# Kernel optimization log

Measured on AMD Instinct MI355X. Metric: run time of the kernel, lower is better.

## Reference

```python
import jax, jax.numpy as jnp
import numpy as np

B, N, C = 8, 1024, 640   # frames, tokens per frame (32x32), channels
H, D = 8, 80             # heads, dim per head; inner = H*D = 640
R = 3                    # adaptive context_range (uniform, odd)
SCALE = D ** -0.5


def _window_indices(batch_size, context_range):
    """Replicates the per-sample index construction in RefAttention.forward.
    First half of the batch attends within [0, B//2-1], second within [B//2, B-1]."""
    half = batch_size // 2
    hr = (context_range - 1) // 2
    rows = []
    for i in range(batch_size):
        lo_b, hi_b = (0, half - 1) if i < half else (half, batch_size - 1)
        ci = list(range(max(lo_b, i - hr), min(hi_b, i + hr + 1)))  # arange(a, min(hi_b, i+hr+1))
        while len(ci) < context_range:
            if ci[0] > lo_b:
                ci = [ci[0] - 1] + ci
            if len(ci) < context_range and ci[-1] < hi_b:
                ci = ci + [ci[-1] + 1]
        rows.append(ci)
    return np.asarray(rows, dtype=np.int32)  # [B, R]


def setup_inputs() -> dict:
    key = jax.random.key(0)
    ks = jax.random.split(key, 6)
    inner = H * D
    x = jax.random.normal(ks[0], (B, N, C), dtype=jnp.float32)
    s = 1.0 / np.sqrt(C)
    Wq = jax.random.normal(ks[1], (inner, C), dtype=jnp.float32) * s
    Wk = jax.random.normal(ks[2], (inner, C), dtype=jnp.float32) * s
    Wv = jax.random.normal(ks[3], (inner, C), dtype=jnp.float32) * s
    Wo = jax.random.normal(ks[4], (C, inner), dtype=jnp.float32) * (1.0 / np.sqrt(inner))
    bo = jnp.zeros((C,), dtype=jnp.float32)
    ctx_idx = jnp.asarray(_window_indices(B, R))  # [B, R] int32, static window gather indices
    return {"x": x, "Wq": Wq, "Wk": Wk, "Wv": Wv, "Wo": Wo, "bo": bo, "ctx_idx": ctx_idx}


def reference(x, Wq, Wk, Wv, Wo, bo, ctx_idx):
    # projections (nn.Linear, no bias): y = x @ W^T
    q = jnp.einsum('bnc,ic->bni', x, Wq)                      # [B, N, inner]
    k = jnp.einsum('bnc,ic->bni', x, Wk)                      # context defaults to x
    v = jnp.einsum('bnc,ic->bni', x, Wv)
    # original uses k.data / v.data (detached); forward value is identical
    qh = q.reshape(B, N, H, D)
    # gather per-frame K/V windows: [B, R, N, inner] -> [B, R*N, H, D]
    kw = k[ctx_idx].reshape(B, R * N, H, D)
    vw = v[ctx_idx].reshape(B, R * N, H, D)
    sim = jnp.einsum('bnhd,bmhd->bhnm', qh, kw) * SCALE       # [B, H, N, R*N]
    attn = jax.nn.softmax(sim, axis=-1)
    out = jnp.einsum('bhnm,bmhd->bnhd', attn, vw).reshape(B, N, H * D)
    return jnp.einsum('bni,ci->bnc', out, Wo) + bo            # to_out (dropout p=0)
```

## Files before the change

### kernel.cpp

```cpp
#include <hip/hip_runtime.h>
#include <hip/hip_bf16.h>

#define BB    8
#define NNTOK 1024
#define CCH   640
#define HH    8
#define DHD   80
#define RRW   3
#define MM    (BB * NNTOK)
#define INNER 640
#define SCALE 0.111803398874989484820458954f
#define QSCALE (SCALE * 1.44269504088896340736f)

#define KSTR 88
#define VSTR 72
#define PSTR 72

typedef __bf16 bf16x8 __attribute__((ext_vector_type(8)));
typedef float  f32x4  __attribute__((ext_vector_type(4)));

__device__ __forceinline__ unsigned short f2b(float f) {
    union { float f; unsigned int u; } v; v.f = f;
    unsigned int r = v.u + 0x7fffu + ((v.u >> 16) & 1u);
    return (unsigned short)(r >> 16);
}
__device__ __forceinline__ bf16x8 zero8() {
    bf16x8 z;
#pragma unroll
    for (int i = 0; i < 8; i++) z[i] = (__bf16)0.0f;
    return z;
}
__device__ __forceinline__ f32x4 zero4() {
    f32x4 z;
#pragma unroll
    for (int i = 0; i < 4; i++) z[i] = 0.0f;
    return z;
}
__device__ __forceinline__ float fexp2(float x) {
#if __has_builtin(__builtin_amdgcn_exp2f)
    return __builtin_amdgcn_exp2f(x);
#else
    return __expf(x * 0.69314718055994530942f);
#endif
}

__global__ __launch_bounds__(256) void castk(const float* __restrict__ s,
                                             unsigned short* __restrict__ d, int n) {
    int i = (blockIdx.x * 256 + threadIdx.x) * 4;
    if (i < n) {
        float4 f = *(const float4*)(s + i);
        ushort4 o;
        o.x = f2b(f.x); o.y = f2b(f.y); o.z = f2b(f.z); o.w = f2b(f.w);
        *(ushort4*)(d + i) = o;
    }
}

__global__ __launch_bounds__(256) void castw4(
    const float* __restrict__ w0, const float* __restrict__ w1,
    const float* __restrict__ w2, const float* __restrict__ w3,
    unsigned short* __restrict__ d0, unsigned short* __restrict__ d1,
    unsigned short* __restrict__ d2, unsigned short* __restrict__ d3, int n)
{
    const float* s; unsigned short* d;
    switch (blockIdx.y) {
        case 0: s = w0; d = d0; break;
        case 1: s = w1; d = d1; break;
        case 2: s = w2; d = d2; break;
        default: s = w3; d = d3; break;
    }
    int i = (blockIdx.x * 256 + threadIdx.x) * 4;
    if (i < n) {
        float4 f = *(const float4*)(s + i);
        ushort4 o;
        o.x = f2b(f.x); o.y = f2b(f.y); o.z = f2b(f.z); o.w = f2b(f.w);
        *(ushort4*)(d + i) = o;
    }
}

__global__ __launch_bounds__(256) void proj_qkv_mfma(
    const unsigned short* __restrict__ xb,
    const unsigned short* __restrict__ wqb,
    const unsigned short* __restrict__ wkb,
    const unsigned short* __restrict__ wvb,
    unsigned short* __restrict__ q16, unsigned short* __restrict__ k16,
    unsigned short* __restrict__ vto)
{
    __shared__ __align__(16) unsigned short Xs[64 * 72];
    __shared__ __align__(16) unsigned short Wsh[64 * 72];
    const int t = threadIdx.x;
    const int wvid = t >> 6, lane = t & 63, col = lane & 15, quad = lane >> 4;
    const int m0 = blockIdx.x * 64, i0 = blockIdx.y * 64, z = blockIdx.z;
    const unsigned short* W = (z == 0) ? wqb : (z == 1) ? wkb : wvb;
    const int row = t >> 2, seg = t & 3;

    f32x4 acc[4];
#pragma unroll
    for (int nt = 0; nt < 4; nt++) acc[nt] = zero4();

    for (int kt = 0; kt < INNER; kt += 64) {
        uint4 x0 = *(const uint4*)(xb + (size_t)(m0 + row) * INNER + kt + seg * 16);
        uint4 x1 = *(const uint4*)(xb + (size_t)(m0 + row) * INNER + kt + seg * 16 + 8);
        uint4 w0 = *(const uint4*)(W  + (size_t)(i0 + row) * INNER + kt + seg * 16);
        uint4 w1 = *(const uint4*)(W  + (size_t)(i0 + row) * INNER + kt + seg * 16 + 8);
        __syncthreads();
        *(uint4*)&Xs[row * 72 + seg * 16]      = x0;
        *(uint4*)&Xs[row * 72 + seg * 16 + 8]  = x1;
        *(uint4*)&Wsh[row * 72 + seg * 16]     = w0;
        *(uint4*)&Wsh[row * 72 + seg * 16 + 8] = w1;
        __syncthreads();
#pragma unroll
        for (int kbk = 0; kbk < 2; kbk++) {
            bf16x8 af = *(const bf16x8*)&Xs[(wvid * 16 + col) * 72 + kbk * 32 + quad * 8];
#pragma unroll
            for (int nt = 0; nt < 4; nt++) {
                bf16x8 bfr = *(const bf16x8*)&Wsh[(nt * 16 + col) * 72 + kbk * 32 + quad * 8];
                acc[nt] = __builtin_amdgcn_mfma_f32_16x16x32_bf16(af, bfr, acc[nt], 0, 0, 0);
            }
        }
    }
    if (z == 0) {
#pragma unroll
        for (int nt = 0; nt < 4; nt++)
#pragma unroll
            for (int r = 0; r < 4; r++)
                q16[(size_t)(m0 + wvid * 16 + quad * 4 + r) * INNER + i0 + nt * 16 + col] = f2b(acc[nt][r] * QSCALE);
    } else if (z == 1) {
#pragma unroll
        for (int nt = 0; nt < 4; nt++)
#pragma unroll
            for (int r = 0; r < 4; r++)
                k16[(size_t)(m0 + wvid * 16 + quad * 4 + r) * INNER + i0 + nt * 16 + col] = f2b(acc[nt][r]);
    } else {
#pragma unroll
        for (int nt = 0; nt < 4; nt++) {
            int i = i0 + nt * 16 + col;
            int h = i / DHD, dd = i % DHD;
#pragma unroll
            for (int r = 0; r < 4; r++) {
                int m = m0 + wvid * 16 + quad * 4 + r;
                int bfm = m >> 10, n = m & (NNTOK - 1);
                vto[((size_t)(bfm * HH + h) * DHD + dd) * NNTOK + n] = f2b(acc[nt][r]);
            }
        }
    }
}

__global__ __launch_bounds__(512, 4) void attn_mfma8(
    const unsigned short* __restrict__ qb, const unsigned short* __restrict__ kb,
    const unsigned short* __restrict__ vt, const int* __restrict__ ctx,
    unsigned short* __restrict__ ao)
{
    __shared__ __align__(16) unsigned short Ks[2][64 * KSTR];
    __shared__ __align__(16) unsigned short Vt[2][DHD * VSTR];
    __shared__ __align__(16) unsigned short Pl[8][16 * PSTR];
    const int t = threadIdx.x;
    const int wvid = t >> 6, lane = t & 63, col = lane & 15, quad = lane >> 4;
    const int qt = blockIdx.x, h = blockIdx.y, b = blockIdx.z;

    bf16x8 qf0, qf1, qf2;
    {
        const unsigned short* qp = qb + (size_t)(b * NNTOK + qt * 128 + wvid * 16 + col) * INNER + h * DHD;
        qf0 = *(const bf16x8*)(qp + quad * 8);
        qf1 = *(const bf16x8*)(qp + 32 + quad * 8);
        qf2 = zero8();
        if (quad < 2) qf2 = *(const bf16x8*)(qp + 64 + quad * 8);
    }
    f32x4 o[5];
#pragma unroll
    for (int dt = 0; dt < 5; dt++) o[dt] = zero4();
    float lp[4];
#pragma unroll
    for (int r = 0; r < 4; r++) lp[r] = 0.0f;
    unsigned short* pw = &Pl[wvid][0];

    const int ki0 = t, ki1 = t + 512;
    const int kkey0 = ki0 / 10, kseg0 = ki0 % 10;
    const int kkey1 = ki1 / 10, kseg1 = ki1 % 10;
    const int vd0 = ki0 >> 3, vs0 = ki0 & 7;
    const int vd1 = ki1 >> 3, vs1 = ki1 & 7;

    {
        const int fr = ctx[b * RRW];
        const unsigned short* kbase = kb + (size_t)(fr * NNTOK) * INNER + h * DHD;
        const unsigned short* vbase = vt + ((size_t)(fr * HH + h) * DHD) * NNTOK;
        uint4 ka0 = *(const uint4*)(kbase + (size_t)kkey0 * INNER + kseg0 * 8);
        uint4 va0 = *(const uint4*)(vbase + (size_t)vd0 * NNTOK + vs0 * 8);
        *(uint4*)&Ks[0][kkey0 * KSTR + kseg0 * 8] = ka0;
        *(uint4*)&Vt[0][vd0 * VSTR + vs0 * 8] = va0;
        if (t < 128) {
            uint4 ka1 = *(const uint4*)(kbase + (size_t)kkey1 * INNER + kseg1 * 8);
            uint4 va1 = *(const uint4*)(vbase + (size_t)vd1 * NNTOK + vs1 * 8);
            *(uint4*)&Ks[0][kkey1 * KSTR + kseg1 * 8] = ka1;
            *(uint4*)&Vt[0][vd1 * VSTR + vs1 * 8] = va1;
        }
    }

    for (int kc = 0; kc < (RRW * NNTOK) / 64; kc++) {
        __syncthreads();

        const int kcn = (kc + 1 < 48) ? kc + 1 : 47;
        const int frn = ctx[b * RRW + (kcn >> 4)];
        const int tokn = (kcn & 15) * 64;
        const unsigned short* kbase = kb + (size_t)(frn * NNTOK + tokn) * INNER + h * DHD;
        const unsigned short* vbase = vt + ((size_t)(frn * HH + h) * DHD) * NNTOK + tokn;
        uint4 ka0 = *(const uint4*)(kbase + (size_t)kkey0 * INNER + kseg0 * 8);
        uint4 va0 = *(const uint4*)(vbase + (size_t)vd0 * NNTOK + vs0 * 8);
        uint4 ka1, va1;
        if (t < 128) {
            ka1 = *(const uint4*)(kbase + (size_t)kkey1 * INNER + kseg1 * 8);
            va1 = *(const uint4*)(vbase + (size_t)vd1 * NNTOK + vs1 * 8);
        }

        const unsigned short* ksr = &Ks[kc & 1][0];
        const unsigned short* vtr = &Vt[kc & 1][0];

        f32x4 s[4];
#pragma unroll
        for (int n0 = 0; n0 < 4; n0++) {
            const unsigned short* kp = ksr + (n0 * 16 + col) * KSTR;
            bf16x8 k0 = *(const bf16x8*)(kp + quad * 8);
            bf16x8 k1 = *(const bf16x8*)(kp + 32 + quad * 8);
            bf16x8 k2 = zero8();
            if (quad < 2) k2 = *(const bf16x8*)(kp + 64 + quad * 8);
            f32x4 sv = zero4();
            sv = __builtin_amdgcn_mfma_f32_16x16x32_bf16(qf0, k0, sv, 0, 0, 0);
            sv = __builtin_amdgcn_mfma_f32_16x16x32_bf16(qf1, k1, sv, 0, 0, 0);
            sv = __builtin_amdgcn_mfma_f32_16x16x32_bf16(qf2, k2, sv, 0, 0, 0);
            s[n0] = sv;
        }
        asm volatile("" ::: "memory");
        __bf16* pb = (__bf16*)pw;
#pragma unroll
        for (int r = 0; r < 4; r++) {
            float p0 = fexp2(s[0][r]), p1 = fexp2(s[1][r]);
            float p2 = fexp2(s[2][r]), p3 = fexp2(s[3][r]);
            lp[r] += (p0 + p1) + (p2 + p3);
            const int rowoff = (quad * 4 + r) * PSTR;
            pb[rowoff +      col] = (__bf16)p0;
            pb[rowoff + 16 + col] = (__bf16)p1;
            pb[rowoff + 32 + col] = (__bf16)p2;
            pb[rowoff + 48 + col] = (__bf16)p3;
        }
        asm volatile("s_waitcnt lgkmcnt(0)" ::: "memory");
        bf16x8 pa0 = *(const bf16x8*)(pw + col * PSTR + quad * 8);
        bf16x8 pa1 = *(const bf16x8*)(pw + col * PSTR + 32 + quad * 8);
#pragma unroll
        for (int dt = 0; dt < 5; dt++) {
            const unsigned short* vp = vtr + (dt * 16 + col) * VSTR;
            bf16x8 v0 = *(const bf16x8*)(vp + quad * 8);
            bf16x8 v1 = *(const bf16x8*)(vp + 32 + quad * 8);
            o[dt] = __builtin_amdgcn_mfma_f32_16x16x32_bf16(pa0, v0, o[dt], 0, 0, 0);
            o[dt] = __builtin_amdgcn_mfma_f32_16x16x32_bf16(pa1, v1, o[dt], 0, 0, 0);
        }
        {
            unsigned short* ksb = &Ks[(kc + 1) & 1][0];
            unsigned short* vtb = &Vt[(kc + 1) & 1][0];
            *(uint4*)&ksb[kkey0 * KSTR + kseg0 * 8] = ka0;
            *(uint4*)&vtb[vd0 * VSTR + vs0 * 8] = va0;
            if (t < 128) {
                *(uint4*)&ksb[kkey1 * KSTR + kseg1 * 8] = ka1;
                *(uint4*)&vtb[vd1 * VSTR + vs1 * 8] = va1;
            }
        }
    }
#pragma unroll
    for (int r = 0; r < 4; r++) {
        float sum = lp[r];
        sum += __shfl_xor(sum, 1);
        sum += __shfl_xor(sum, 2);
        sum += __shfl_xor(sum, 4);
        sum += __shfl_xor(sum, 8);
        lp[r] = sum;
    }
#pragma unroll
    for (int r = 0; r < 4; r++) {
        const float inv = 1.0f / lp[r];
        unsigned short* op = ao + (size_t)(b * NNTOK + qt * 128 + wvid * 16 + quad * 4 + r) * INNER + h * DHD;
#pragma unroll
        for (int dt = 0; dt < 5; dt++)
            op[dt * 16 + col] = f2b(o[dt][r] * inv);
    }
}

__global__ __launch_bounds__(256) void proj_out_mfma(
    const unsigned short* __restrict__ ab, const unsigned short* __restrict__ wob,
    const float* __restrict__ bo, float* __restrict__ out)
{
    __shared__ __align__(16) unsigned short Xs[64 * 72];
    __shared__ __align__(16) unsigned short Wsh[64 * 72];
    const int t = threadIdx.x;
    const int wvid = t >> 6, lane = t & 63, col = lane & 15, quad = lane >> 4;
    const int m0 = blockIdx.x * 64, i0 = blockIdx.y * 64;
    const int row = t >> 2, seg = t & 3;

    float bias[4];
#pragma unroll
    for (int nt = 0; nt < 4; nt++) bias[nt] = bo[i0 + nt * 16 + col];

    f32x4 acc[4];
#pragma unroll
    for (int nt = 0; nt < 4; nt++) acc[nt] = zero4();

    for (int kt = 0; kt < INNER; kt += 64) {
        uint4 x0 = *(const uint4*)(ab  + (size_t)(m0 + row) * INNER + kt + seg * 16);
        uint4 x1 = *(const uint4*)(ab  + (size_t)(m0 + row) * INNER + kt + seg * 16 + 8);
        uint4 w0 = *(const uint4*)(wob + (size_t)(i0 + row) * INNER + kt + seg * 16);
        uint4 w1 = *(const uint4*)(wob + (size_t)(i0 + row) * INNER + kt + seg * 16 + 8);
        __syncthreads();
        *(uint4*)&Xs[row * 72 + seg * 16]      = x0;
        *(uint4*)&Xs[row * 72 + seg * 16 + 8]  = x1;
        *(uint4*)&Wsh[row * 72 + seg * 16]     = w0;
        *(uint4*)&Wsh[row * 72 + seg * 16 + 8] = w1;
        __syncthreads();
#pragma unroll
        for (int kbk = 0; kbk < 2; kbk++) {
            bf16x8 af = *(const bf16x8*)&Xs[(wvid * 16 + col) * 72 + kbk * 32 + quad * 8];
#pragma unroll
            for (int nt = 0; nt < 4; nt++) {
                bf16x8 bfr = *(const bf16x8*)&Wsh[(nt * 16 + col) * 72 + kbk * 32 + quad * 8];
                acc[nt] = __builtin_amdgcn_mfma_f32_16x16x32_bf16(af, bfr, acc[nt], 0, 0, 0);
            }
        }
    }
#pragma unroll
    for (int nt = 0; nt < 4; nt++)
#pragma unroll
        for (int r = 0; r < 4; r++)
            out[(size_t)(m0 + wvid * 16 + quad * 4 + r) * CCH + i0 + nt * 16 + col] = acc[nt][r] + bias[nt];
}

extern "C" void kernel_launch(void* const* d_in, const int* in_sizes, int n_in,
                              void* d_out, int out_size, void* d_ws, size_t ws_size,
                              hipStream_t stream) {
    const float* x  = (const float*)d_in[0];
    const float* wq = (const float*)d_in[1];
    const float* wk = (const float*)d_in[2];
    const float* wv = (const float*)d_in[3];
    const float* wo = (const float*)d_in[4];
    const float* bo = (const float*)d_in[5];
    const int* ctx  = (const int*)d_in[6];
    float* out = (float*)d_out;

    const size_t XN = (size_t)MM * INNER;
    const size_t WN = (size_t)INNER * CCH;
    unsigned short* q16 = (unsigned short*)d_ws;
    unsigned short* k16 = q16 + XN;
    unsigned short* vto = k16 + XN;
    unsigned short* xb  = vto + XN;
    unsigned short* aob = xb;
    unsigned short* wqb = xb + XN;
    unsigned short* wkb = wqb + WN;
    unsigned short* wvb = wkb + WN;
    unsigned short* wob = wvb + WN;

    castk<<<dim3((XN / 4 + 255) / 256), 256, 0, stream>>>(x, xb, (int)XN);
    castw4<<<dim3((WN / 4 + 255) / 256, 4), 256, 0, stream>>>(wq, wk, wv, wo, wqb, wkb, wvb, wob, (int)WN);

    proj_qkv_mfma<<<dim3(MM / 64, INNER / 64, 3), 256, 0, stream>>>(xb, wqb, wkb, wvb, q16, k16, vto);
    attn_mfma8<<<dim3(NNTOK / 128, HH, BB), 512, 0, stream>>>(q16, k16, vto, ctx, aob);
    proj_out_mfma<<<dim3(MM / 64, CCH / 64), 256, 0, stream>>>(aob, wob, bo, out);
}
```

Measured before the change: 242.7 us.

## Keep attention probabilities in registers via transposed S MFMA and permuted K layout

Swaps the MFMA operand order so each lane holds S-transposed values, and permutes the K rows in shared memory so that the exp'd scores already sit in the A-operand layout of the P·V MFMA. This removes the per-wave LDS round trip for P, its waitcnt and its shared-memory footprint. Row sums are now accumulated per lane and reduced with cross-quad shuffles at the end. The risk is that the index permutation must exactly match the MFMA register layout for correctness.

```diff
diff --git a/kernel.cpp b/kernel.cpp
--- a/kernel.cpp
+++ b/kernel.cpp
@@ -14,7 +14,6 @@
 
 #define KSTR 88
 #define VSTR 72
-#define PSTR 72
 
 typedef __bf16 bf16x8 __attribute__((ext_vector_type(8)));
 typedef float  f32x4  __attribute__((ext_vector_type(4)));
@@ -145,14 +144,17 @@
     }
 }
 
-__global__ __launch_bounds__(512, 4) void attn_mfma8(
+__device__ __forceinline__ int ksrow(int tau) {
+    return (((tau >> 5) * 2 + ((tau >> 2) & 1)) << 4) + (((tau >> 3) & 3) << 2) + (tau & 3);
+}
+
+__global__ __launch_bounds__(512, 4) void attn_mfma9(
     const unsigned short* __restrict__ qb, const unsigned short* __restrict__ kb,
     const unsigned short* __restrict__ vt, const int* __restrict__ ctx,
     unsigned short* __restrict__ ao)
 {
     __shared__ __align__(16) unsigned short Ks[2][64 * KSTR];
     __shared__ __align__(16) unsigned short Vt[2][DHD * VSTR];
-    __shared__ __align__(16) unsigned short Pl[8][16 * PSTR];
     const int t = threadIdx.x;
     const int wvid = t >> 6, lane = t & 63, col = lane & 15, quad = lane >> 4;
     const int qt = blockIdx.x, h = blockIdx.y, b = blockIdx.z;
@@ -168,14 +170,12 @@
     f32x4 o[5];
 #pragma unroll
     for (int dt = 0; dt < 5; dt++) o[dt] = zero4();
-    float lp[4];
-#pragma unroll
-    for (int r = 0; r < 4; r++) lp[r] = 0.0f;
-    unsigned short* pw = &Pl[wvid][0];
+    float lp = 0.0f;
 
     const int ki0 = t, ki1 = t + 512;
-    const int kkey0 = ki0 / 10, kseg0 = ki0 % 10;
-    const int kkey1 = ki1 / 10, kseg1 = ki1 % 10;
+    const int ktok0 = ki0 / 10, kseg0 = ki0 % 10;
+    const int ktok1 = ki1 / 10, kseg1 = ki1 % 10;
+    const int ksr0 = ksrow(ktok0), ksr1 = ksrow(ktok1);
     const int vd0 = ki0 >> 3, vs0 = ki0 & 7;
     const int vd1 = ki1 >> 3, vs1 = ki1 & 7;
 
@@ -183,14 +183,14 @@
         const int fr = ctx[b * RRW];
         const unsigned short* kbase = kb + (size_t)(fr * NNTOK) * INNER + h * DHD;
         const unsigned short* vbase = vt + ((size_t)(fr * HH + h) * DHD) * NNTOK;
-        uint4 ka0 = *(const uint4*)(kbase + (size_t)kkey0 * INNER + kseg0 * 8);
+        uint4 ka0 = *(const uint4*)(kbase + (size_t)ktok0 * INNER + kseg0 * 8);
         uint4 va0 = *(const uint4*)(vbase + (size_t)vd0 * NNTOK + vs0 * 8);
-        *(uint4*)&Ks[0][kkey0 * KSTR + kseg0 * 8] = ka0;
+        *(uint4*)&Ks[0][ksr0 * KSTR + kseg0 * 8] = ka0;
         *(uint4*)&Vt[0][vd0 * VSTR + vs0 * 8] = va0;
         if (t < 128) {
-            uint4 ka1 = *(const uint4*)(kbase + (size_t)kkey1 * INNER + kseg1 * 8);
+            uint4 ka1 = *(const uint4*)(kbase + (size_t)ktok1 * INNER + kseg1 * 8);
             uint4 va1 = *(const uint4*)(vbase + (size_t)vd1 * NNTOK + vs1 * 8);
-            *(uint4*)&Ks[0][kkey1 * KSTR + kseg1 * 8] = ka1;
+            *(uint4*)&Ks[0][ksr1 * KSTR + kseg1 * 8] = ka1;
             *(uint4*)&Vt[0][vd1 * VSTR + vs1 * 8] = va1;
         }
     }
@@ -203,11 +203,11 @@
         const int tokn = (kcn & 15) * 64;
         const unsigned short* kbase = kb + (size_t)(frn * NNTOK + tokn) * INNER + h * DHD;
         const unsigned short* vbase = vt + ((size_t)(frn * HH + h) * DHD) * NNTOK + tokn;
-        uint4 ka0 = *(const uint4*)(kbase + (size_t)kkey0 * INNER + kseg0 * 8);
+        uint4 ka0 = *(const uint4*)(kbase + (size_t)ktok0 * INNER + kseg0 * 8);
         uint4 va0 = *(const uint4*)(vbase + (size_t)vd0 * NNTOK + vs0 * 8);
         uint4 ka1, va1;
         if (t < 128) {
-            ka1 = *(const uint4*)(kbase + (size_t)kkey1 * INNER + kseg1 * 8);
+            ka1 = *(const uint4*)(kbase + (size_t)ktok1 * INNER + kseg1 * 8);
             va1 = *(const uint4*)(vbase + (size_t)vd1 * NNTOK + vs1 * 8);
         }
 
@@ -223,27 +223,29 @@
             bf16x8 k2 = zero8();
             if (quad < 2) k2 = *(const bf16x8*)(kp + 64 + quad * 8);
             f32x4 sv = zero4();
-            sv = __builtin_amdgcn_mfma_f32_16x16x32_bf16(qf0, k0, sv, 0, 0, 0);
-            sv = __builtin_amdgcn_mfma_f32_16x16x32_bf16(qf1, k1, sv, 0, 0, 0);
-            sv = __builtin_amdgcn_mfma_f32_16x16x32_bf16(qf2, k2, sv, 0, 0, 0);
+            sv = __builtin_amdgcn_mfma_f32_16x16x32_bf16(k0, qf0, sv, 0, 0, 0);
+            sv = __builtin_amdgcn_mfma_f32_16x16x32_bf16(k1, qf1, sv, 0, 0, 0);
+            sv = __builtin_amdgcn_mfma_f32_16x16x32_bf16(k2, qf2, sv, 0, 0, 0);
             s[n0] = sv;
         }
-        asm volatile("" ::: "memory");
-        __bf16* pb = (__bf16*)pw;
-#pragma unroll
-        for (int r = 0; r < 4; r++) {
-            float p0 = fexp2(s[0][r]), p1 = fexp2(s[1][r]);
-            float p2 = fexp2(s[2][r]), p3 = fexp2(s[3][r]);
-            lp[r] += (p0 + p1) + (p2 + p3);
-            const int rowoff = (quad * 4 + r) * PSTR;
-            pb[rowoff +      col] = (__bf16)p0;
-            pb[rowoff + 16 + col] = (__bf16)p1;
-            pb[rowoff + 32 + col] = (__bf16)p2;
-            pb[rowoff + 48 + col] = (__bf16)p3;
-        }
-        asm volatile("s_waitcnt lgkmcnt(0)" ::: "memory");
-        bf16x8 pa0 = *(const bf16x8*)(pw + col * PSTR + quad * 8);
-        bf16x8 pa1 = *(const bf16x8*)(pw + col * PSTR + 32 + quad * 8);
+        bf16x8 pa0, pa1;
+        float l0 = 0.0f, l1 = 0.0f;
+#pragma unroll
+        for (int n0 = 0; n0 < 4; n0++) {
+            float p0 = fexp2(s[n0][0]), p1 = fexp2(s[n0][1]);
+            float p2 = fexp2(s[n0][2]), p3 = fexp2(s[n0][3]);
+            if (n0 < 2) l0 += (p0 + p1) + (p2 + p3);
+            else        l1 += (p0 + p1) + (p2 + p3);
+            const int j0 = (n0 & 1) * 4;
+            if (n0 < 2) {
+                pa0[j0]     = (__bf16)p0; pa0[j0 + 1] = (__bf16)p1;
+                pa0[j0 + 2] = (__bf16)p2; pa0[j0 + 3] = (__bf16)p3;
+            } else {
+                pa1[j0]     = (__bf16)p0; pa1[j0 + 1] = (__bf16)p1;
+                pa1[j0 + 2] = (__bf16)p2; pa1[j0 + 3] = (__bf16)p3;
+            }
+        }
+        lp += l0 + l1;
 #pragma unroll
         for (int dt = 0; dt < 5; dt++) {
             const unsigned short* vp = vtr + (dt * 16 + col) * VSTR;
@@ -255,30 +257,27 @@
         {
             unsigned short* ksb = &Ks[(kc + 1) & 1][0];
             unsigned short* vtb = &Vt[(kc + 1) & 1][0];
-            *(uint4*)&ksb[kkey0 * KSTR + kseg0 * 8] = ka0;
+            *(uint4*)&ksb[ksr0 * KSTR + kseg0 * 8] = ka0;
             *(uint4*)&vtb[vd0 * VSTR + vs0 * 8] = va0;
             if (t < 128) {
-                *(uint4*)&ksb[kkey1 * KSTR + kseg1 * 8] = ka1;
+                *(uint4*)&ksb[ksr1 * KSTR + kseg1 * 8] = ka1;
                 *(uint4*)&vtb[vd1 * VSTR + vs1 * 8] = va1;
             }
         }
     }
+    float lsum = lp;
+    lsum += __shfl_xor(lsum, 16);
+    lsum += __shfl_xor(lsum, 32);
+    float inv[4];
+#pragma unroll
+    for (int r = 0; r < 4; r++)
+        inv[r] = 1.0f / __shfl(lsum, quad * 4 + r);
 #pragma unroll
     for (int r = 0; r < 4; r++) {
-        float sum = lp[r];
-        sum += __shfl_xor(sum, 1);
-        sum += __shfl_xor(sum, 2);
-        sum += __shfl_xor(sum, 4);
-        sum += __shfl_xor(sum, 8);
-        lp[r] = sum;
-    }
-#pragma unroll
-    for (int r = 0; r < 4; r++) {
-        const float inv = 1.0f / lp[r];
         unsigned short* op = ao + (size_t)(b * NNTOK + qt * 128 + wvid * 16 + quad * 4 + r) * INNER + h * DHD;
 #pragma unroll
         for (int dt = 0; dt < 5; dt++)
-            op[dt * 16 + col] = f2b(o[dt][r] * inv);
+            op[dt * 16 + col] = f2b(o[dt][r] * inv[r]);
     }
 }
 
@@ -357,6 +356,6 @@
     castw4<<<dim3((WN / 4 + 255) / 256, 4), 256, 0, stream>>>(wq, wk, wv, wo, wqb, wkb, wvb, wob, (int)WN);
 
     proj_qkv_mfma<<<dim3(MM / 64, INNER / 64, 3), 256, 0, stream>>>(xb, wqb, wkb, wvb, q16, k16, vto);
-    attn_mfma8<<<dim3(NNTOK / 128, HH, BB), 512, 0, stream>>>(q16, k16, vto, ctx, aob);
+    attn_mfma9<<<dim3(NNTOK / 128, HH, BB), 512, 0, stream>>>(q16, k16, vto, ctx, aob);
     proj_out_mfma<<<dim3(MM / 64, CCH / 64), 256, 0, stream>>>(aob, wob, bo, out);
 }
```

After: 224.3 us. 7.6% less time.
